# Performance work log

Hardware: AMD Instinct MI355X
Metric: run time of the kernel (lower is better)

The kernel has to match this reference:

```python
import jax, jax.numpy as jnp
import numpy as np

N = 100000      # n_nodes
E = 1000000     # n_edges (avg degree 10)
D = 64          # input feature dim
LAT = 7         # latent_dim
R = 2           # perturb_rank
H = 2 * LAT     # GCN hidden / dense1 width = 14
P = (LAT + 1) * R  # dense2 width = 16
SP_INV_1 = float(np.log(np.expm1(1.0)))  # softplus_inverse(1.0)


def setup_inputs() -> dict:
    key = jax.random.key(0)
    ks = jax.random.split(key, 10)
    X = jax.random.normal(ks[0], (N, D), dtype=jnp.float32)
    rows = jax.random.randint(ks[1], (E,), 0, N, dtype=jnp.int32)
    cols = jax.random.randint(ks[2], (E,), 0, N, dtype=jnp.int32)
    vals = jax.random.uniform(ks[3], (E,), dtype=jnp.float32)
    s = 0.1
    W1 = jax.random.normal(ks[4], (D, H), dtype=jnp.float32) * s
    W2 = jax.random.normal(ks[5], (H, H), dtype=jnp.float32) * s
    Wd1 = jax.random.normal(ks[6], (H, H), dtype=jnp.float32) * s
    bd1 = jnp.zeros((H,), jnp.float32)
    Wd2 = jax.random.normal(ks[7], (H, P), dtype=jnp.float32) * s
    bd2 = jnp.zeros((P,), jnp.float32)
    return dict(X=X, rows=rows, cols=cols, vals=vals, W1=W1, W2=W2,
                Wd1=Wd1, bd1=bd1, Wd2=Wd2, bd2=bd2)


def reference(X, rows, cols, vals, W1, W2, Wd1, bd1, Wd2, bd2):
    # Sparse adjacency SpMM: (A @ F)[i] = sum_e vals[e] * F[cols[e]] for rows[e]==i
    def spmm(F):
        gathered = vals[:, None] * F[cols]          # [E, d] irregular gather
        return jax.ops.segment_sum(gathered, rows, num_segments=N)

    # GraphConvolution: relu(A @ X @ W)  (keras-gcn order: aggregate then transform)
    h = jax.nn.relu(spmm(X) @ W1)                   # [N, 14]
    h = jax.nn.relu(spmm(h) @ W2)                   # [N, 14]

    param_dist = jnp.tanh(h @ Wd1 + bd1)            # [N, 14]
    param_perturb = jnp.tanh(h @ Wd2 + bd2)         # [N, 16]

    loc = param_dist[:, :LAT]                                      # [N, 7]
    scale_diag = jax.nn.softplus(param_dist[:, LAT:] + SP_INV_1)   # [N, 7]
    perturb_U = param_perturb[:, :LAT * R]                         # [N, 14] (-> [N,7,2])
    perturb_m = param_perturb[:, LAT * R:]                         # [N, 2]

    # MVN-diag-plus-low-rank parameters, concatenated: [N, 7+7+14+2]
    return jnp.concatenate([loc, scale_diag, perturb_U, perturb_m], axis=-1)
```

## Files before the change

kernel.cpp:

```cpp
#include <hip/hip_runtime.h>
#include <hip/hip_fp16.h>
#include <math.h>

constexpr int D     = 64;
constexpr int H     = 14;
constexpr int HP2   = 8;
constexpr int P     = 16;
constexpr int LATc  = 7;
constexpr int OUTW  = 30;
constexpr float SP_INV_1 = 0.5413248546129181f;

__device__ __forceinline__ void pk_atomic_add_f16(__half2* addr, __half2 val) {
    unsigned int bits = *reinterpret_cast<unsigned int*>(&val);
    asm volatile("global_atomic_pk_add_f16 %0, %1, off"
                 :: "v"(addr), "v"(bits) : "memory");
}

__global__ void dense_xw_kernel(const float* __restrict__ X,
                                const float* __restrict__ W1,
                                __half2* __restrict__ XW,
                                __half2* __restrict__ Y1,
                                __half2* __restrict__ Y2, int N) {
    __shared__ float w[D * H];
    for (int i = threadIdx.x; i < D * H; i += blockDim.x) w[i] = W1[i];
    __syncthreads();
    int t = blockIdx.x * blockDim.x + threadIdx.x;
    int n = t >> 1;
    int half = t & 1;
    if (n >= N) return;

    float acc[H];
#pragma unroll
    for (int j = 0; j < H; ++j) acc[j] = 0.f;
    const float4* xr = reinterpret_cast<const float4*>(X + (size_t)n * D) + half * 8;
#pragma unroll
    for (int d4 = 0; d4 < 8; ++d4) {
        float4 x = xr[d4];
        float xs[4] = {x.x, x.y, x.z, x.w};
#pragma unroll
        for (int k = 0; k < 4; ++k) {
            int d = half * 32 + d4 * 4 + k;
#pragma unroll
            for (int j = 0; j < H; ++j) acc[j] = fmaf(xs[k], w[d * H + j], acc[j]);
        }
    }
#pragma unroll
    for (int j = 0; j < H; ++j) acc[j] += __shfl_xor(acc[j], 1);

    __half2 ov[4];
    if (half == 0) {
        ov[0] = __floats2half2_rn(acc[0], acc[1]);
        ov[1] = __floats2half2_rn(acc[2], acc[3]);
        ov[2] = __floats2half2_rn(acc[4], acc[5]);
        ov[3] = __floats2half2_rn(acc[6], acc[7]);
    } else {
        ov[0] = __floats2half2_rn(acc[8], acc[9]);
        ov[1] = __floats2half2_rn(acc[10], acc[11]);
        ov[2] = __floats2half2_rn(acc[12], acc[13]);
        ov[3] = __floats2half2_rn(0.f, 0.f);
    }
    reinterpret_cast<float4*>(XW + (size_t)n * HP2)[half] = *reinterpret_cast<float4*>(ov);
    float4 z = make_float4(0.f, 0.f, 0.f, 0.f);
    reinterpret_cast<float4*>(Y1 + (size_t)n * HP2)[half] = z;
    reinterpret_cast<float4*>(Y2 + (size_t)n * HP2)[half] = z;
}

__global__ void spmm_pk_kernel(const __half2* __restrict__ F,
                               const int* __restrict__ rows,
                               const int* __restrict__ cols,
                               const float* __restrict__ vals,
                               __half2* __restrict__ Y, int E) {
    int idx = blockIdx.x * blockDim.x + threadIdx.x;
    int e = idx >> 3;
    int f = idx & 7;
    if (e >= E || f >= 7) return;
    int r = rows[e];
    int c = cols[e];
    float v = vals[e];
    float2 xf = __half22float2(F[c * HP2 + f]);
    __half2 p = __floats2half2_rn(v * xf.x, v * xf.y);
    pk_atomic_add_f16(&Y[r * HP2 + f], p);
}

__global__ void spmm_relu_kernel(const __half2* __restrict__ Y1,
                                 const int* __restrict__ rows,
                                 const int* __restrict__ cols,
                                 const float* __restrict__ vals,
                                 __half2* __restrict__ Y2, int E) {
    int idx = blockIdx.x * blockDim.x + threadIdx.x;
    int e = idx >> 3;
    int f = idx & 7;
    if (e >= E || f >= 7) return;
    int r = rows[e];
    int c = cols[e];
    float v = vals[e];
    float2 xf = __half22float2(Y1[c * HP2 + f]);
    __half2 p = __floats2half2_rn(v * fmaxf(xf.x, 0.f), v * fmaxf(xf.y, 0.f));
    pk_atomic_add_f16(&Y2[r * HP2 + f], p);
}

__global__ __launch_bounds__(256) void final_kernel(
        const __half2* __restrict__ Z,
        const float* __restrict__ W2,
        const float* __restrict__ Wd1,
        const float* __restrict__ bd1,
        const float* __restrict__ Wd2,
        const float* __restrict__ bd2,
        float* __restrict__ out, int N) {
    __shared__ float w2[H * H], wd1[H * H], wd2[H * P], b1[H], b2[P];
    __shared__ float so[256 * OUTW];
    for (int i = threadIdx.x; i < H * H; i += 256) { w2[i] = W2[i]; wd1[i] = Wd1[i]; }
    for (int i = threadIdx.x; i < H * P; i += 256) wd2[i] = Wd2[i];
    if (threadIdx.x < H) b1[threadIdx.x] = bd1[threadIdx.x];
    if (threadIdx.x < P) b2[threadIdx.x] = bd2[threadIdx.x];
    __syncthreads();

    int base = blockIdx.x * 256;
    int n = base + threadIdx.x;
    if (n < N) {
        const float4* zr4 = reinterpret_cast<const float4*>(Z + (size_t)n * HP2);
        float4 za = zr4[0], zb = zr4[1];
        __half2 zh[HP2];
        *reinterpret_cast<float4*>(&zh[0]) = za;
        *reinterpret_cast<float4*>(&zh[4]) = zb;
        float z[H];
#pragma unroll
        for (int k = 0; k < 7; ++k) {
            float2 t = __half22float2(zh[k]);
            z[2 * k]     = t.x;
            z[2 * k + 1] = t.y;
        }
        float h[H];
#pragma unroll
        for (int j = 0; j < H; ++j) {
            float a = 0.f;
#pragma unroll
            for (int i = 0; i < H; ++i) a = fmaf(z[i], w2[i * H + j], a);
            h[j] = fmaxf(a, 0.f);
        }
        float* so_row = &so[threadIdx.x * OUTW];
        float pd7[LATc];
#pragma unroll
        for (int j = 0; j < H; ++j) {
            float a = b1[j];
#pragma unroll
            for (int i = 0; i < H; ++i) a = fmaf(h[i], wd1[i * H + j], a);
            float t = tanhf(a);
            if (j < LATc) so_row[j] = t;
            else pd7[j - LATc] = t;
        }
#pragma unroll
        for (int k = 0; k < LATc; ++k) {
            float x = pd7[k] + SP_INV_1;
            so_row[LATc + k] = log1pf(expf(x));
        }
#pragma unroll
        for (int j = 0; j < P; ++j) {
            float a = b2[j];
#pragma unroll
            for (int i = 0; i < H; ++i) a = fmaf(h[i], wd2[i * P + j], a);
            so_row[14 + j] = tanhf(a);
        }
    }
    __syncthreads();

    int rowsHere = N - base;
    if (rowsHere > 256) rowsHere = 256;
    if (rowsHere < 0) rowsHere = 0;
    int cnt = rowsHere * OUTW;
    float* obase = out + (size_t)base * OUTW;
    for (int i = threadIdx.x; i < cnt; i += 256) obase[i] = so[i];
}

extern "C" void kernel_launch(void* const* d_in, const int* in_sizes, int n_in,
                              void* d_out, int out_size, void* d_ws, size_t ws_size,
                              hipStream_t stream) {
    const float* X    = (const float*)d_in[0];
    const int*   rows = (const int*)d_in[1];
    const int*   cols = (const int*)d_in[2];
    const float* vals = (const float*)d_in[3];
    const float* W1   = (const float*)d_in[4];
    const float* W2   = (const float*)d_in[5];
    const float* Wd1  = (const float*)d_in[6];
    const float* bd1  = (const float*)d_in[7];
    const float* Wd2  = (const float*)d_in[8];
    const float* bd2  = (const float*)d_in[9];
    float* out = (float*)d_out;

    const int N = in_sizes[0] / D;
    const int E = in_sizes[1];

    __half2* XW = (__half2*)d_ws;
    __half2* Y1 = XW + (size_t)N * HP2;
    __half2* Y2 = Y1 + (size_t)N * HP2;

    int blkN  = (N + 255) / 256;
    int blkN2 = (2 * N + 255) / 256;
    long long spmmThreads = (long long)E * 8;
    unsigned blkS = (unsigned)((spmmThreads + 255) / 256);

    dense_xw_kernel<<<blkN2, 256, 0, stream>>>(X, W1, XW, Y1, Y2, N);
    spmm_pk_kernel<<<blkS, 256, 0, stream>>>(XW, rows, cols, vals, Y1, E);
    spmm_relu_kernel<<<blkS, 256, 0, stream>>>(Y1, rows, cols, vals, Y2, E);
    final_kernel<<<blkN, 256, 0, stream>>>(Y2, W2, Wd1, bd1, Wd2, bd2, out, N);
}
```

Baseline: 218.4 us.

## Fuse both SpMM passes into one persistent kernel with a grid barrier

Replaces the two separate SpMM kernel launches with a single persistent grid-stride kernel sized to full occupancy. The two passes are separated by a software grid-wide barrier built on an atomic counter, which the dense kernel resets. This removes one launch and the drain/ramp gap between the passes. In exchange it adds spin-wait cost, relies on every block being co-resident (otherwise it deadlocks), and uses a grid-stride loop instead of one thread per element.

```diff
diff --git a/kernel.cpp b/kernel.cpp
--- a/kernel.cpp
+++ b/kernel.cpp
@@ -9,6 +9,7 @@
 constexpr int LATc  = 7;
 constexpr int OUTW  = 30;
 constexpr float SP_INV_1 = 0.5413248546129181f;
+constexpr int BLK   = 256;
 
 __device__ __forceinline__ void pk_atomic_add_f16(__half2* addr, __half2 val) {
     unsigned int bits = *reinterpret_cast<unsigned int*>(&val);
@@ -16,11 +17,25 @@
                  :: "v"(addr), "v"(bits) : "memory");
 }
 
+__device__ __forceinline__ void grid_bar(int* ctr, int target) {
+    __syncthreads();
+    if (threadIdx.x == 0) {
+        __threadfence();
+        __hip_atomic_fetch_add(ctr, 1, __ATOMIC_RELAXED, __HIP_MEMORY_SCOPE_AGENT);
+        while (__hip_atomic_load(ctr, __ATOMIC_RELAXED, __HIP_MEMORY_SCOPE_AGENT) < target)
+            __builtin_amdgcn_s_sleep(2);
+        __threadfence();
+    }
+    __syncthreads();
+}
+
 __global__ void dense_xw_kernel(const float* __restrict__ X,
                                 const float* __restrict__ W1,
                                 __half2* __restrict__ XW,
                                 __half2* __restrict__ Y1,
-                                __half2* __restrict__ Y2, int N) {
+                                __half2* __restrict__ Y2,
+                                int* __restrict__ bar, int N) {
+    if (blockIdx.x == 0 && threadIdx.x < 8) bar[threadIdx.x] = 0;
     __shared__ float w[D * H];
     for (int i = threadIdx.x; i < D * H; i += blockDim.x) w[i] = W1[i];
     __syncthreads();
@@ -65,38 +80,42 @@
     reinterpret_cast<float4*>(Y2 + (size_t)n * HP2)[half] = z;
 }
 
-__global__ void spmm_pk_kernel(const __half2* __restrict__ F,
-                               const int* __restrict__ rows,
-                               const int* __restrict__ cols,
-                               const float* __restrict__ vals,
-                               __half2* __restrict__ Y, int E) {
-    int idx = blockIdx.x * blockDim.x + threadIdx.x;
-    int e = idx >> 3;
-    int f = idx & 7;
-    if (e >= E || f >= 7) return;
-    int r = rows[e];
-    int c = cols[e];
-    float v = vals[e];
-    float2 xf = __half22float2(F[c * HP2 + f]);
-    __half2 p = __floats2half2_rn(v * xf.x, v * xf.y);
-    pk_atomic_add_f16(&Y[r * HP2 + f], p);
-}
-
-__global__ void spmm_relu_kernel(const __half2* __restrict__ Y1,
-                                 const int* __restrict__ rows,
-                                 const int* __restrict__ cols,
-                                 const float* __restrict__ vals,
-                                 __half2* __restrict__ Y2, int E) {
-    int idx = blockIdx.x * blockDim.x + threadIdx.x;
-    int e = idx >> 3;
-    int f = idx & 7;
-    if (e >= E || f >= 7) return;
-    int r = rows[e];
-    int c = cols[e];
-    float v = vals[e];
-    float2 xf = __half22float2(Y1[c * HP2 + f]);
-    __half2 p = __floats2half2_rn(v * fmaxf(xf.x, 0.f), v * fmaxf(xf.y, 0.f));
-    pk_atomic_add_f16(&Y2[r * HP2 + f], p);
+__global__ __launch_bounds__(BLK, 8) void spmm2x_kernel(
+        const __half2* __restrict__ XW,
+        const int* __restrict__ rows,
+        const int* __restrict__ cols,
+        const float* __restrict__ vals,
+        __half2* __restrict__ Y1,
+        __half2* __restrict__ Y2,
+        int* __restrict__ bar,
+        int E, int nblk) {
+    const int tid = blockIdx.x * BLK + threadIdx.x;
+    const int nth = gridDim.x * BLK;
+    const long long tot = (long long)E * 8;
+
+    for (long long i = tid; i < tot; i += nth) {
+        int e = (int)(i >> 3), f = (int)(i & 7);
+        if (f < 7) {
+            int r = rows[e], c = cols[e];
+            float v = vals[e];
+            float2 xf = __half22float2(XW[c * HP2 + f]);
+            __half2 p = __floats2half2_rn(v * xf.x, v * xf.y);
+            pk_atomic_add_f16(&Y1[r * HP2 + f], p);
+        }
+    }
+
+    grid_bar(bar, nblk);
+
+    for (long long i = tid; i < tot; i += nth) {
+        int e = (int)(i >> 3), f = (int)(i & 7);
+        if (f < 7) {
+            int r = rows[e], c = cols[e];
+            float v = vals[e];
+            float2 xf = __half22float2(Y1[c * HP2 + f]);
+            __half2 p = __floats2half2_rn(v * fmaxf(xf.x, 0.f), v * fmaxf(xf.y, 0.f));
+            pk_atomic_add_f16(&Y2[r * HP2 + f], p);
+        }
+    }
 }
 
 __global__ __launch_bounds__(256) void final_kernel(
@@ -193,14 +212,21 @@
     __half2* XW = (__half2*)d_ws;
     __half2* Y1 = XW + (size_t)N * HP2;
     __half2* Y2 = Y1 + (size_t)N * HP2;
+    int* bar = (int*)(Y2 + (size_t)N * HP2);
+
+    int blocksPerCU = 0;
+    (void)hipOccupancyMaxActiveBlocksPerMultiprocessor(
+        &blocksPerCU, (const void*)spmm2x_kernel, BLK, 0);
+    int numCU = 0;
+    (void)hipDeviceGetAttribute(&numCU, hipDeviceAttributeMultiprocessorCount, 0);
+    int grid = (blocksPerCU > 0 && numCU > 0) ? blocksPerCU * numCU : 1024;
+    if (grid > 4096) grid = 4096;
 
     int blkN  = (N + 255) / 256;
     int blkN2 = (2 * N + 255) / 256;
-    long long spmmThreads = (long long)E * 8;
-    unsigned blkS = (unsigned)((spmmThreads + 255) / 256);
-
-    dense_xw_kernel<<<blkN2, 256, 0, stream>>>(X, W1, XW, Y1, Y2, N);
-    spmm_pk_kernel<<<blkS, 256, 0, stream>>>(XW, rows, cols, vals, Y1, E);
-    spmm_relu_kernel<<<blkS, 256, 0, stream>>>(Y1, rows, cols, vals, Y2, E);
+
+    dense_xw_kernel<<<blkN2, 256, 0, stream>>>(X, W1, XW, Y1, Y2, bar, N);
+    spmm2x_kernel<<<grid, BLK, 0, stream>>>(XW, rows, cols, vals, Y1, Y2,
+                                            bar, E, grid);
     final_kernel<<<blkN, 256, 0, stream>>>(Y2, W2, Wd1, bd1, Wd2, bd2, out, N);
 }
```

Result: slower. 448.6 us (+105.4%).
